# Kernel tuning notes

Hardware: AMD Instinct MI355X
Metric: run time of the kernel (lower is better)

## Reference

```python
import jax, jax.numpy as jnp
import numpy as np

GRID_N = 3   # number of grid intervals (pykan 'grid')
K = 3        # spline order (pykan 'k')
IN_F = 512
OUT_F = 512
BATCH = 8
SEQ = 2048


def _extended_grid(d, dtype):
    # base grid: num+1 points over [-1, 1]; extend by K steps of h on each side (pykan extend_grid)
    pts = jnp.linspace(-1.0, 1.0, GRID_N + 1).astype(dtype)
    h = jnp.asarray(2.0 / GRID_N, dtype)
    left = pts[0] + h * jnp.arange(-K, 0, dtype=dtype)
    right = pts[-1] + h * jnp.arange(1, K + 1, dtype=dtype)
    ext = jnp.concatenate([left, pts, right])           # (GRID_N + 1 + 2K,)
    return jnp.broadcast_to(ext, (d, ext.shape[0]))     # per-input-feature grid (shared values)


def _bspline_basis(x, grid):
    # Cox-de Boor recursion, vectorized over tokens and input features.
    # x: (N, D), grid: (D, M) -> returns (N, D, M-1-K) = (N, D, GRID_N+K)
    x = x[:, :, None]                     # (N, D, 1)
    g = grid[None, :, :]                  # (1, D, M)
    B = ((x >= g[..., :-1]) & (x < g[..., 1:])).astype(x.dtype)
    for p in range(1, K + 1):
        left = (x - g[..., :-(p + 1)]) / (g[..., p:-1] - g[..., :-(p + 1)])
        right = (g[..., p + 1:] - x) / (g[..., p + 1:] - g[..., 1:-p])
        B = left * B[..., :-1] + right * B[..., 1:]
    return B


def setup_inputs() -> dict:
    key = jax.random.key(0)
    k1, k2, k3 = jax.random.split(key, 3)
    x = jax.random.normal(k1, (BATCH, SEQ, IN_F), dtype=jnp.float32)
    coef = jax.random.normal(k2, (OUT_F, IN_F, GRID_N + K), dtype=jnp.float32) * 0.1
    scale_base = (1.0 / np.sqrt(IN_F)) + (jax.random.uniform(k3, (OUT_F, IN_F), dtype=jnp.float32) * 2.0 - 1.0) * 0.1
    scale_sp = jnp.ones((OUT_F, IN_F), dtype=jnp.float32)
    bias = jnp.zeros((OUT_F,), dtype=jnp.float32)
    return {"x": x, "coef": coef, "scale_base": scale_base, "scale_sp": scale_sp, "bias": bias}


def reference(x, coef, scale_base, scale_sp, bias):
    B_, S, D = x.shape
    xf = x.reshape(-1, D)                               # (N, D) tokens
    grid = _extended_grid(D, xf.dtype)
    basis = _bspline_basis(xf, grid)                    # (N, D, GRID_N+K)
    base = jax.nn.silu(xf)                              # base activation per input feature
    # per-edge: scale_base*silu(x_i) + scale_sp*spline(x_i); sum over input features, add bias
    spline_w = scale_sp[..., None] * coef               # (O, D, GRID_N+K)
    y = (jnp.einsum('ni,oi->no', base, scale_base)
         + jnp.einsum('nib,oib->no', basis, spline_w)
         + bias[None, :])
    return y.reshape(B_, S, -1)
```

## Files before the change

### kernel.cpp

```cpp
#include <hip/hip_runtime.h>


typedef short        bf16x8 __attribute__((ext_vector_type(8)));
typedef float        f32x4  __attribute__((ext_vector_type(4)));
typedef unsigned int u32x4  __attribute__((ext_vector_type(4)));

#define NROWS 16384
#define DIN   512
#define DOUT  512
#define BM    64
#define BN    512
#define NKT   64

__device__ __forceinline__ unsigned short f2bf(float f) {
    unsigned int u = __float_as_uint(f);
    u += 0x7fffu + ((u >> 16) & 1u);
    return (unsigned short)(u >> 16);
}

__device__ __forceinline__ u32x4 kan_act(float xv) {
    float S  = __builtin_fmaf(xv, 1.5f, 4.5f);
    float jf = floorf(S);
    float t  = S - jf;
    int   j  = (int)jf;
    float t2 = t * t;
    float t3 = t2 * t;
    float omt  = 1.0f - t;
    float omt2 = omt * omt;
    float n0 = omt2 * omt * (1.0f / 6.0f);
    float n1 = __builtin_fmaf(t3, 0.5f, -t2) + (2.0f / 3.0f);
    float u  = (t + t2) - t3;
    float n2 = __builtin_fmaf(u, 0.5f, 1.0f / 6.0f);
    float n3 = t3 * (1.0f / 6.0f);
    float e  = __expf(-xv);
    float si = xv * __builtin_amdgcn_rcpf(1.0f + e);

    unsigned P01, P23, WS;
    asm("v_cvt_pk_bf16_f32 %0, %1, %2" : "=v"(P01) : "v"(n0), "v"(n1));
    asm("v_cvt_pk_bf16_f32 %0, %1, %2" : "=v"(P23) : "v"(n2), "v"(n3));
    asm("v_cvt_pk_bf16_f32 %0, %1, %2" : "=v"(WS)  : "v"(si), "v"(0.0f));
    unsigned U = P01 << 16;
    unsigned V = (P01 >> 16) | (P23 << 16);
    unsigned Z = P23 >> 16;
    bool odd = (j & 1) != 0;
    unsigned c0 = odd ? U : P01;
    unsigned c1 = odd ? V : P23;
    unsigned c2 = odd ? Z : 0u;
    int b = (j - 2) >> 1;
    u32x4 w;
    w[0] = (b == 0) ? c0 : (b == -1) ? c1 : (b == -2) ? c2 : 0u;
    w[1] = (b == 1) ? c0 : (b ==  0) ? c1 : (b == -1) ? c2 : 0u;
    w[2] = (b == 2) ? c0 : (b ==  1) ? c1 : (b ==  0) ? c2 : 0u;
    w[3] = (b == 3) ? c0 : (b ==  2) ? c1 : (b ==  1) ? c2 : 0u;
    w[0] = (w[0] & 0xFFFF0000u) | (WS & 0xFFFFu);
    return w;
}

__global__ __launch_bounds__(256) void kan_prep(
    const float* __restrict__ coef, const float* __restrict__ scale_base,
    const float* __restrict__ scale_sp, unsigned short* __restrict__ wt)
{
    int t = blockIdx.x * 256 + threadIdx.x;
    int o = t >> 9;
    int i = t & 511;
    float sb = scale_base[t];
    float sp = scale_sp[t];
    const float* cp = coef + (size_t)t * 6;
    bf16x8 w;
    w[0] = (short)f2bf(sb);
#pragma unroll
    for (int b = 0; b < 6; ++b) w[1 + b] = (short)f2bf(sp * cp[b]);
    w[7] = 0;
    int kt = i >> 3, s = i & 7, ks = s >> 2, fg = s & 3;
    size_t off = ((size_t)((kt * 2 + ks) * 512 + o)) * 64 + fg * 16;
    *(bf16x8*)((char*)wt + off) = w;
}

__global__ __launch_bounds__(512, 2) void kan_gemm(
    const float* __restrict__ x, const unsigned short* __restrict__ wt,
    const float* __restrict__ bias, float* __restrict__ y)
{
    __shared__ char As[2][BM * 128];

    const int tid  = threadIdx.x;
    const int lane = tid & 63;
    const int wid  = tid >> 6;

    int bid = blockIdx.x;
    int mt  = (bid & 7) * 32 + (bid >> 3);
    const int row0 = mt * BM;

    const int ar = tid >> 3;
    const int ap = tid & 7;
    const float* xp = x + (size_t)(row0 + ar) * DIN + ap;
    const int as_sw = (ar & 7) << 4;
    const int c0 = ap << 4;

    const int fr = lane & 15;
    const int fg = lane >> 4;

    const unsigned asb =
        (unsigned)(unsigned long long)(__attribute__((address_space(3))) char*)&As[0][0];

    const char* pB[4];
#pragma unroll
    for (int n2 = 0; n2 < 4; ++n2)
        pB[n2] = (const char*)wt + (size_t)((wid * 64 + n2 * 16 + fr) * 64 + fg * 16);

    f32x4 acc[4][4];
#pragma unroll
    for (int m2 = 0; m2 < 4; ++m2)
#pragma unroll
        for (int n2 = 0; n2 < 4; ++n2) {
            f32x4 z = {0.f, 0.f, 0.f, 0.f};
            acc[m2][n2] = z;
        }

    bf16x8 Ba[8], Bb[8];
    float  xA, xB;

    {
        float x0 = xp[0];
        u32x4 w0 = kan_act(x0);
        unsigned woff = asb + ar * 128 + (c0 ^ as_sw);
        asm volatile("ds_write_b128 %0, %1" :: "v"(woff), "v"(w0));
    }
#pragma unroll
    for (int q = 0; q < 8; ++q) {
        int n2_ = q & 3, ks_ = q >> 2;
        const void* a_ = pB[n2_] + ks_ * 32768;
        asm volatile("global_load_dwordx4 %0, %1, off" : "=&v"(Ba[q]) : "v"(a_));
    }
    asm volatile("global_load_dword %0, %1, off"
                 : "=&v"(xA) : "v"((const void*)(xp + 8)));
    asm volatile("s_waitcnt lgkmcnt(0)");
    __builtin_amdgcn_s_barrier();

#define STEP(ktv, Bc, Bn, xcur, xnext)                                        \
    {                                                                         \
        const int cur_ = (ktv) & 1;                                           \
        const unsigned abase_ = asb + cur_ * 8192;                            \
        bf16x8 AF[8];                                                         \
        _Pragma("unroll")                                                     \
        for (int q = 0; q < 8; ++q) {                                         \
            int ks_ = q >> 2, m2_ = q & 3;                                    \
            int rr_ = m2_ * 16 + fr;                                          \
            unsigned off_ = abase_ + rr_ * 128                                \
                + ((unsigned)(ks_ * 64 + fg * 16) ^ (unsigned)((rr_ & 7) << 4)); \
            asm volatile("ds_read_b128 %0, %1" : "=&v"(AF[q]) : "v"(off_));   \
        }                                                                     \
        const bool hn_ = (ktv) + 1 < NKT;                                     \
        if (hn_) {                                                            \
            size_t ko_ = (size_t)((ktv) + 1) * 65536;                         \
            _Pragma("unroll")                                                 \
            for (int q = 0; q < 8; ++q) {                                     \
                int n2_ = q & 3, ks_ = q >> 2;                                \
                const void* a_ = pB[n2_] + ko_ + ks_ * 32768;                 \
                asm volatile("global_load_dwordx4 %0, %1, off"                \
                             : "=&v"(Bn[q]) : "v"(a_));                       \
            }                                                                 \
            int xo_ = ((ktv) + 2 < NKT) ? ((ktv) + 2) * 8 : 0;                \
            asm volatile("global_load_dword %0, %1, off"                      \
                         : "=&v"(xnext) : "v"((const void*)(xp + xo_)));      \
            asm volatile("s_waitcnt vmcnt(9)");                               \
        } else {                                                              \
            asm volatile("s_waitcnt vmcnt(0)");                               \
        }                                                                     \
        __builtin_amdgcn_sched_barrier(0);                                    \
        if (hn_) {                                                            \
            u32x4 w_ = kan_act(xcur);                                         \
            unsigned woff_ = asb + (cur_ ^ 1) * 8192 + ar * 128 + (c0 ^ as_sw); \
            asm volatile("ds_write_b128 %0, %1" :: "v"(woff_), "v"(w_));      \
            asm volatile("s_waitcnt lgkmcnt(1)");                             \
        } else {                                                              \
            asm volatile("s_waitcnt lgkmcnt(0)");                             \
        }                                                                     \
        __builtin_amdgcn_sched_barrier(0);                                    \
        _Pragma("unroll")                                                     \
        for (int ks_ = 0; ks_ < 2; ++ks_)                                     \
            _Pragma("unroll")                                                 \
            for (int m2_ = 0; m2_ < 4; ++m2_)                                 \
                _Pragma("unroll")                                             \
                for (int n2_ = 0; n2_ < 4; ++n2_)                             \
                    acc[m2_][n2_] = __builtin_amdgcn_mfma_f32_16x16x32_bf16(  \
                        AF[ks_ * 4 + m2_], Bc[ks_ * 4 + n2_], acc[m2_][n2_],  \
                        0, 0, 0);                                             \
        if (hn_) {                                                            \
            asm volatile("s_waitcnt lgkmcnt(0)");                             \
            __builtin_amdgcn_s_barrier();                                     \
        }                                                                     \
    }

    for (int kt = 0; kt < NKT; kt += 2) {
        STEP(kt,     Ba, Bb, xA, xB);
        STEP(kt + 1, Bb, Ba, xB, xA);
    }

    const int orow0 = row0 + fg * 4;
    const int ocol0 = wid * 64 + fr;
#pragma unroll
    for (int n2 = 0; n2 < 4; ++n2) {
        float bv = bias[ocol0 + n2 * 16];
#pragma unroll
        for (int m2 = 0; m2 < 4; ++m2) {
#pragma unroll
            for (int r = 0; r < 4; ++r) {
                y[(size_t)(orow0 + m2 * 16 + r) * DOUT + (ocol0 + n2 * 16)]
                    = acc[m2][n2][r] + bv;
            }
        }
    }
#undef STEP
}

extern "C" void kernel_launch(void* const* d_in, const int* in_sizes, int n_in,
                              void* d_out, int out_size, void* d_ws, size_t ws_size,
                              hipStream_t stream)
{
    const float* x          = (const float*)d_in[0];
    const float* coef       = (const float*)d_in[1];
    const float* scale_base = (const float*)d_in[2];
    const float* scale_sp   = (const float*)d_in[3];
    const float* bias       = (const float*)d_in[4];
    unsigned short* wt = (unsigned short*)d_ws;
    float* y = (float*)d_out;

    kan_prep<<<1024, 256, 0, stream>>>(coef, scale_base, scale_sp, wt);
    kan_gemm<<<256, 512, 0, stream>>>(x, wt, bias, y);
}
```

Measured before the change: 78.88 us.

## Deepen A-tile pipeline with 4-stage LDS ring and register double-buffered fragments

Expands the shared-memory A buffer from 2 to 4 stages and prefetches the next step's A fragments from LDS into a second register set while MFMAs consume the current set. The activation for tile kt+2 is written two stages ahead, so LDS reads no longer sit at the head of each step waiting before the MFMAs start. In exchange it doubles LDS use per block and adds 8 bf16x8 registers per thread, which may hurt occupancy under launch_bounds(512,2). There is also a risk in the wait counts: the new LDS reads are issued before the vmcnt wait and the final lgkmcnt(0) still covers them.

```diff
diff --git a/kernel.cpp b/kernel.cpp
--- a/kernel.cpp
+++ b/kernel.cpp
@@ -80,7 +80,7 @@
     const float* __restrict__ x, const unsigned short* __restrict__ wt,
     const float* __restrict__ bias, float* __restrict__ y)
 {
-    __shared__ char As[2][BM * 128];
+    __shared__ char As[4][BM * 128];
 
     const int tid  = threadIdx.x;
     const int lane = tid & 63;
@@ -117,13 +117,15 @@
         }
 
     bf16x8 Ba[8], Bb[8];
+    bf16x8 AFa[8], AFb[8];
     float  xA, xB;
 
     {
-        float x0 = xp[0];
-        u32x4 w0 = kan_act(x0);
-        unsigned woff = asb + ar * 128 + (c0 ^ as_sw);
-        asm volatile("ds_write_b128 %0, %1" :: "v"(woff), "v"(w0));
+        u32x4 w0 = kan_act(xp[0]);
+        unsigned o0 = asb + ar * 128 + (c0 ^ as_sw);
+        asm volatile("ds_write_b128 %0, %1" :: "v"(o0), "v"(w0));
+        u32x4 w1 = kan_act(xp[8]);
+        asm volatile("ds_write_b128 %0, %1" :: "v"(o0 + 8192), "v"(w1));
     }
 #pragma unroll
     for (int q = 0; q < 8; ++q) {
@@ -132,23 +134,21 @@
         asm volatile("global_load_dwordx4 %0, %1, off" : "=&v"(Ba[q]) : "v"(a_));
     }
     asm volatile("global_load_dword %0, %1, off"
-                 : "=&v"(xA) : "v"((const void*)(xp + 8)));
+                 : "=&v"(xA) : "v"((const void*)(xp + 16)));
     asm volatile("s_waitcnt lgkmcnt(0)");
     __builtin_amdgcn_s_barrier();
-
-#define STEP(ktv, Bc, Bn, xcur, xnext)                                        \
+#pragma unroll
+    for (int q = 0; q < 8; ++q) {
+        int ks_ = q >> 2, m2_ = q & 3;
+        int rr_ = m2_ * 16 + fr;
+        unsigned off_ = asb + rr_ * 128
+            + ((unsigned)(ks_ * 64 + fg * 16) ^ (unsigned)((rr_ & 7) << 4));
+        asm volatile("ds_read_b128 %0, %1" : "=&v"(AFa[q]) : "v"(off_));
+    }
+    asm volatile("s_waitcnt lgkmcnt(0)");
+
+#define STEP(ktv, Bc, Bn, AFc, AFn, xcur, xnext)                              \
     {                                                                         \
-        const int cur_ = (ktv) & 1;                                           \
-        const unsigned abase_ = asb + cur_ * 8192;                            \
-        bf16x8 AF[8];                                                         \
-        _Pragma("unroll")                                                     \
-        for (int q = 0; q < 8; ++q) {                                         \
-            int ks_ = q >> 2, m2_ = q & 3;                                    \
-            int rr_ = m2_ * 16 + fr;                                          \
-            unsigned off_ = abase_ + rr_ * 128                                \
-                + ((unsigned)(ks_ * 64 + fg * 16) ^ (unsigned)((rr_ & 7) << 4)); \
-            asm volatile("ds_read_b128 %0, %1" : "=&v"(AF[q]) : "v"(off_));   \
-        }                                                                     \
         const bool hn_ = (ktv) + 1 < NKT;                                     \
         if (hn_) {                                                            \
             size_t ko_ = (size_t)((ktv) + 1) * 65536;                         \
@@ -159,21 +159,29 @@
                 asm volatile("global_load_dwordx4 %0, %1, off"                \
                              : "=&v"(Bn[q]) : "v"(a_));                       \
             }                                                                 \
-            int xo_ = ((ktv) + 2 < NKT) ? ((ktv) + 2) * 8 : 0;                \
+            int xo_ = ((ktv) + 3 < NKT) ? ((ktv) + 3) * 8 : 0;                \
             asm volatile("global_load_dword %0, %1, off"                      \
                          : "=&v"(xnext) : "v"((const void*)(xp + xo_)));      \
+            const unsigned abn_ = asb + (((ktv) + 1) & 3) * 8192;             \
+            _Pragma("unroll")                                                 \
+            for (int q = 0; q < 8; ++q) {                                     \
+                int ks_ = q >> 2, m2_ = q & 3;                                \
+                int rr_ = m2_ * 16 + fr;                                      \
+                unsigned off_ = abn_ + rr_ * 128                              \
+                    + ((unsigned)(ks_ * 64 + fg * 16)                         \
+                       ^ (unsigned)((rr_ & 7) << 4));                         \
+                asm volatile("ds_read_b128 %0, %1" : "=&v"(AFn[q]) : "v"(off_)); \
+            }                                                                 \
             asm volatile("s_waitcnt vmcnt(9)");                               \
         } else {                                                              \
             asm volatile("s_waitcnt vmcnt(0)");                               \
         }                                                                     \
         __builtin_amdgcn_sched_barrier(0);                                    \
-        if (hn_) {                                                            \
+        if ((ktv) + 2 < NKT) {                                                \
             u32x4 w_ = kan_act(xcur);                                         \
-            unsigned woff_ = asb + (cur_ ^ 1) * 8192 + ar * 128 + (c0 ^ as_sw); \
-            asm volatile("ds_write_b128 %0, %1" :: "v"(woff_), "v"(w_));      \
-            asm volatile("s_waitcnt lgkmcnt(1)");                             \
-        } else {                                                              \
-            asm volatile("s_waitcnt lgkmcnt(0)");                             \
+            unsigned wo_ = asb + (((ktv) + 2) & 3) * 8192 + ar * 128          \
+                           + (c0 ^ as_sw);                                    \
+            asm volatile("ds_write_b128 %0, %1" :: "v"(wo_), "v"(w_));        \
         }                                                                     \
         __builtin_amdgcn_sched_barrier(0);                                    \
         _Pragma("unroll")                                                     \
@@ -183,7 +191,7 @@
                 _Pragma("unroll")                                             \
                 for (int n2_ = 0; n2_ < 4; ++n2_)                             \
                     acc[m2_][n2_] = __builtin_amdgcn_mfma_f32_16x16x32_bf16(  \
-                        AF[ks_ * 4 + m2_], Bc[ks_ * 4 + n2_], acc[m2_][n2_],  \
+                        AFc[ks_ * 4 + m2_], Bc[ks_ * 4 + n2_], acc[m2_][n2_], \
                         0, 0, 0);                                             \
         if (hn_) {                                                            \
             asm volatile("s_waitcnt lgkmcnt(0)");                             \
@@ -192,8 +200,8 @@
     }
 
     for (int kt = 0; kt < NKT; kt += 2) {
-        STEP(kt,     Ba, Bb, xA, xB);
-        STEP(kt + 1, Bb, Ba, xB, xA);
+        STEP(kt,     Ba, Bb, AFa, AFb, xA, xB);
+        STEP(kt + 1, Bb, Ba, AFb, AFa, xB, xA);
     }
 
     const int orow0 = row0 + fg * 4;
```

Measured after the change: 83.71 us. 1.06x slower.

## Split MFMA k-steps to overlap activation compute and use SGPR-based addressing

Applied to the files above, without the earlier changes.

Addressing changes: weight and x loads now use a precomputed 32-bit VGPR offset plus a scalar base, and LDS reads and writes fold the double-buffer select into immediate offsets. Both cut per-iteration VALU address arithmetic. The schedule also changes: the first half of the MFMAs runs as soon as half the A fragments are ready, then the spline activation and LDS write for the next tile run, then the second MFMA half. This hides the activation compute behind matrix work. The risk is that the new waitcnt thresholds are wrong, or that pressure on the memory queue changes.

```diff
diff --git a/kernel.cpp b/kernel.cpp
--- a/kernel.cpp
+++ b/kernel.cpp
@@ -92,7 +92,6 @@
 
     const int ar = tid >> 3;
     const int ap = tid & 7;
-    const float* xp = x + (size_t)(row0 + ar) * DIN + ap;
     const int as_sw = (ar & 7) << 4;
     const int c0 = ap << 4;
 
@@ -102,10 +101,24 @@
     const unsigned asb =
         (unsigned)(unsigned long long)(__attribute__((address_space(3))) char*)&As[0][0];
 
-    const char* pB[4];
-#pragma unroll
-    for (int n2 = 0; n2 < 4; ++n2)
-        pB[n2] = (const char*)wt + (size_t)((wid * 64 + n2 * 16 + fr) * 64 + fg * 16);
+    unsigned voffB[8];
+#pragma unroll
+    for (int q = 0; q < 8; ++q) {
+        int n2_ = q & 3, ks_ = q >> 2;
+        voffB[q] = (unsigned)((wid * 64 + n2_ * 16 + fr) * 64 + fg * 16
+                              + ks_ * 32768);
+    }
+    unsigned afoff[8];
+#pragma unroll
+    for (int q = 0; q < 8; ++q) {
+        int ks_ = q >> 2, m2_ = q & 3;
+        int rr_ = m2_ * 16 + fr;
+        afoff[q] = asb + (unsigned)(rr_ * 128)
+                 + (((unsigned)(ks_ * 64 + fg * 16)) ^ ((unsigned)((rr_ & 7) << 4)));
+    }
+    const unsigned awoff = asb + (unsigned)(ar * 128) + (unsigned)(c0 ^ as_sw);
+    const unsigned vxoff = (unsigned)((ar * DIN + ap) * 4);
+    const char* xrow = (const char*)(x + (size_t)row0 * DIN);
 
     f32x4 acc[4][4];
 #pragma unroll
@@ -120,71 +133,62 @@
     float  xA, xB;
 
     {
-        float x0 = xp[0];
-        u32x4 w0 = kan_act(x0);
-        unsigned woff = asb + ar * 128 + (c0 ^ as_sw);
-        asm volatile("ds_write_b128 %0, %1" :: "v"(woff), "v"(w0));
-    }
-#pragma unroll
-    for (int q = 0; q < 8; ++q) {
-        int n2_ = q & 3, ks_ = q >> 2;
-        const void* a_ = pB[n2_] + ks_ * 32768;
-        asm volatile("global_load_dwordx4 %0, %1, off" : "=&v"(Ba[q]) : "v"(a_));
-    }
-    asm volatile("global_load_dword %0, %1, off"
-                 : "=&v"(xA) : "v"((const void*)(xp + 8)));
+        u32x4 w0 = kan_act(*(const float*)(xrow + vxoff));
+        asm volatile("ds_write_b128 %0, %1" :: "v"(awoff), "v"(w0));
+    }
+#pragma unroll
+    for (int q = 0; q < 8; ++q)
+        asm volatile("global_load_dwordx4 %0, %1, %2"
+                     : "=&v"(Ba[q]) : "v"(voffB[q]), "s"((const void*)wt));
+    asm volatile("global_load_dword %0, %1, %2"
+                 : "=&v"(xA) : "v"(vxoff), "s"((const void*)(xrow + 1 * 32)));
     asm volatile("s_waitcnt lgkmcnt(0)");
     __builtin_amdgcn_s_barrier();
 
-#define STEP(ktv, Bc, Bn, xcur, xnext)                                        \
+#define STEP(ktv, CUR, Bc, Bn, xcur, xnext)                                   \
     {                                                                         \
-        const int cur_ = (ktv) & 1;                                           \
-        const unsigned abase_ = asb + cur_ * 8192;                            \
+        const bool hn_ = (ktv) + 1 < NKT;                                     \
         bf16x8 AF[8];                                                         \
         _Pragma("unroll")                                                     \
-        for (int q = 0; q < 8; ++q) {                                         \
-            int ks_ = q >> 2, m2_ = q & 3;                                    \
-            int rr_ = m2_ * 16 + fr;                                          \
-            unsigned off_ = abase_ + rr_ * 128                                \
-                + ((unsigned)(ks_ * 64 + fg * 16) ^ (unsigned)((rr_ & 7) << 4)); \
-            asm volatile("ds_read_b128 %0, %1" : "=&v"(AF[q]) : "v"(off_));   \
-        }                                                                     \
-        const bool hn_ = (ktv) + 1 < NKT;                                     \
+        for (int q = 0; q < 8; ++q)                                           \
+            asm volatile("ds_read_b128 %0, %1 offset:%c2"                     \
+                         : "=&v"(AF[q]) : "v"(afoff[q]), "i"((CUR) * 8192));  \
         if (hn_) {                                                            \
-            size_t ko_ = (size_t)((ktv) + 1) * 65536;                         \
+            const void* wb1_ = (const char*)wt + (size_t)((ktv) + 1) * 65536; \
             _Pragma("unroll")                                                 \
-            for (int q = 0; q < 8; ++q) {                                     \
-                int n2_ = q & 3, ks_ = q >> 2;                                \
-                const void* a_ = pB[n2_] + ko_ + ks_ * 32768;                 \
-                asm volatile("global_load_dwordx4 %0, %1, off"                \
-                             : "=&v"(Bn[q]) : "v"(a_));                       \
-            }                                                                 \
-            int xo_ = ((ktv) + 2 < NKT) ? ((ktv) + 2) * 8 : 0;                \
-            asm volatile("global_load_dword %0, %1, off"                      \
-                         : "=&v"(xnext) : "v"((const void*)(xp + xo_)));      \
-            asm volatile("s_waitcnt vmcnt(9)");                               \
+            for (int q = 0; q < 8; ++q)                                       \
+                asm volatile("global_load_dwordx4 %0, %1, %2"                 \
+                             : "=&v"(Bn[q]) : "v"(voffB[q]), "s"(wb1_));      \
+            int xk_ = ((ktv) + 2 < NKT) ? ((ktv) + 2) : 0;                    \
+            asm volatile("global_load_dword %0, %1, %2"                       \
+                         : "=&v"(xnext)                                       \
+                         : "v"(vxoff), "s"((const void*)(xrow + xk_ * 32)));  \
+            asm volatile("s_waitcnt vmcnt(14) lgkmcnt(4)");                   \
         } else {                                                              \
-            asm volatile("s_waitcnt vmcnt(0)");                               \
-        }                                                                     \
-        __builtin_amdgcn_sched_barrier(0);                                    \
-        if (hn_) {                                                            \
-            u32x4 w_ = kan_act(xcur);                                         \
-            unsigned woff_ = asb + (cur_ ^ 1) * 8192 + ar * 128 + (c0 ^ as_sw); \
-            asm volatile("ds_write_b128 %0, %1" :: "v"(woff_), "v"(w_));      \
-            asm volatile("s_waitcnt lgkmcnt(1)");                             \
-        } else {                                                              \
-            asm volatile("s_waitcnt lgkmcnt(0)");                             \
+            asm volatile("s_waitcnt vmcnt(0) lgkmcnt(0)");                    \
         }                                                                     \
         __builtin_amdgcn_sched_barrier(0);                                    \
         _Pragma("unroll")                                                     \
-        for (int ks_ = 0; ks_ < 2; ++ks_)                                     \
+        for (int m2_ = 0; m2_ < 4; ++m2_)                                     \
             _Pragma("unroll")                                                 \
-            for (int m2_ = 0; m2_ < 4; ++m2_)                                 \
-                _Pragma("unroll")                                             \
-                for (int n2_ = 0; n2_ < 4; ++n2_)                             \
-                    acc[m2_][n2_] = __builtin_amdgcn_mfma_f32_16x16x32_bf16(  \
-                        AF[ks_ * 4 + m2_], Bc[ks_ * 4 + n2_], acc[m2_][n2_],  \
-                        0, 0, 0);                                             \
+            for (int n2_ = 0; n2_ < 4; ++n2_)                                 \
+                acc[m2_][n2_] = __builtin_amdgcn_mfma_f32_16x16x32_bf16(      \
+                    AF[m2_], Bc[n2_], acc[m2_][n2_], 0, 0, 0);                \
+        if (hn_) {                                                            \
+            asm volatile("s_waitcnt vmcnt(9)");                               \
+            __builtin_amdgcn_sched_barrier(0);                                \
+            u32x4 w_ = kan_act(xcur);                                         \
+            asm volatile("ds_write_b128 %0, %1 offset:%c2"                    \
+                         :: "v"(awoff), "v"(w_), "i"(((CUR) ^ 1) * 8192));    \
+            asm volatile("s_waitcnt lgkmcnt(1)");                             \
+        }                                                                     \
+        __builtin_amdgcn_sched_barrier(0);                                    \
+        _Pragma("unroll")                                                     \
+        for (int m2_ = 0; m2_ < 4; ++m2_)                                     \
+            _Pragma("unroll")                                                 \
+            for (int n2_ = 0; n2_ < 4; ++n2_)                                 \
+                acc[m2_][n2_] = __builtin_amdgcn_mfma_f32_16x16x32_bf16(      \
+                    AF[4 + m2_], Bc[4 + n2_], acc[m2_][n2_], 0, 0, 0);        \
         if (hn_) {                                                            \
             asm volatile("s_waitcnt lgkmcnt(0)");                             \
             __builtin_amdgcn_s_barrier();                                     \
@@ -192,8 +196,8 @@
     }
 
     for (int kt = 0; kt < NKT; kt += 2) {
-        STEP(kt,     Ba, Bb, xA, xB);
-        STEP(kt + 1, Bb, Ba, xB, xA);
+        STEP(kt,     0, Ba, Bb, xA, xB);
+        STEP(kt + 1, 1, Bb, Ba, xB, xA);
     }
 
     const int orow0 = row0 + fg * 4;
```

Result: no change. 78.32 us (-0.7%).
